# Performance work log

Measured on AMD Instinct MI355X. Metric: run time of the kernel, lower is better.

The kernel has to match this reference:

```python
import jax, jax.numpy as jnp
import numpy as np

N_NODES = 100000
N_EDGES = 3200000
NFEAT = 256
NHID = 256


def setup_inputs() -> dict:
    key = jax.random.key(0)
    k_x, k_ws, k_wn, k_src, k_dst = jax.random.split(key, 5)
    x = jax.random.normal(k_x, (N_NODES, NFEAT), dtype=jnp.float32)
    W_self = jax.random.normal(k_ws, (NFEAT, NHID), dtype=jnp.float32) * (1.0 / np.sqrt(NFEAT))
    W_neigh = jax.random.normal(k_wn, (NFEAT, NHID), dtype=jnp.float32) * (1.0 / np.sqrt(NFEAT))
    b = jnp.zeros((NHID,), dtype=jnp.float32)
    edge_src = jax.random.randint(k_src, (N_EDGES,), 0, N_NODES, dtype=jnp.int32)
    edge_dst = jax.random.randint(k_dst, (N_EDGES,), 0, N_NODES, dtype=jnp.int32)
    return {"x": x, "W_self": W_self, "W_neigh": W_neigh, "b": b,
            "edge_src": edge_src, "edge_dst": edge_dst}


def reference(x, W_self, W_neigh, b, edge_src, edge_dst):
    n = x.shape[0]
    # mean aggregation over incoming edges: gather src feats, scatter-add to dst
    msg = x[edge_src]                                              # [E, F]
    agg = jax.ops.segment_sum(msg, edge_dst, num_segments=n)       # [N, F]
    deg = jax.ops.segment_sum(jnp.ones_like(edge_dst, dtype=x.dtype),
                              edge_dst, num_segments=n)            # [N]
    h_neigh = agg / jnp.maximum(deg, 1.0)[:, None]                 # mean (0 for isolated)
    # SAGEConv 'mean': fc_self(x) + fc_neigh(h_neigh) (bias on neigh branch)
    out = x @ W_self + h_neigh @ W_neigh + b                       # [N, H]
    return jax.nn.relu(out)
```

## Files before the change

### kernel.cpp

```cpp
#include <hip/hip_runtime.h>
#include <stdint.h>

typedef __attribute__((ext_vector_type(8))) short bf16x8;
typedef __attribute__((ext_vector_type(4))) float f32x4;
typedef __attribute__((ext_vector_type(2))) float f32x2;

#define NF 256
#define NH 256
#define KTOT 512
#define BM 128
#define BK 64
#define EB 512
#define NBIN 512

static __device__ __forceinline__ unsigned short f2bf(float f){
  union { float f; unsigned int u; } v; v.f = f;
  unsigned int r = v.u + 0x7fffu + ((v.u >> 16) & 1u);
  return (unsigned short)(r >> 16);
}
static __device__ __forceinline__ unsigned int f2e4(float f){
  union { float f; unsigned int u; } v; v.f = f;
  unsigned int s = v.u >> 31;
  unsigned int mag = v.u & 0x7fffffffu;
  if (mag > 0x43E00000u) mag = 0x43E00000u;
  unsigned int r = mag + 0x7ffffu + ((mag >> 20) & 1u);
  if (r < 0x3C800000u) return 0u;
  return (s << 7) | (((r >> 20) - 960u) & 0x7fu);
}
static __device__ __forceinline__ ushort4 dec8(unsigned int v){
#if __has_builtin(__builtin_amdgcn_cvt_pk_f32_fp8)
  f32x2 lo = __builtin_amdgcn_cvt_pk_f32_fp8((int)v, false);
  f32x2 hi = __builtin_amdgcn_cvt_pk_f32_fp8((int)v, true);
  ushort4 o; o.x=f2bf(lo[0]); o.y=f2bf(lo[1]); o.z=f2bf(hi[0]); o.w=f2bf(hi[1]);
  return o;
#else
  ushort4 o; unsigned short r[4];
  #pragma unroll
  for (int j = 0; j < 4; j++){
    unsigned int b = (v >> (8*j)) & 0xffu;
    unsigned int tt = b & 0x7fu;
    union { unsigned int u; float f; } w;
    w.u = ((tt + 960u) << 20) | ((b & 0x80u) << 24);
    r[j] = tt ? f2bf(w.f) : (unsigned short)0;
  }
  o.x=r[0]; o.y=r[1]; o.z=r[2]; o.w=r[3];
  return o;
#endif
}
static __device__ __forceinline__ void accw(unsigned int v, f32x2& a, f32x2& b){
#if __has_builtin(__builtin_amdgcn_cvt_pk_f32_fp8)
  a += __builtin_amdgcn_cvt_pk_f32_fp8((int)v, false);
  b += __builtin_amdgcn_cvt_pk_f32_fp8((int)v, true);
#else
  #pragma unroll
  for (int j = 0; j < 4; j++){
    unsigned int bb = (v >> (8*j)) & 0xffu;
    unsigned int tt = bb & 0x7fu;
    union { unsigned int u; float f; } w;
    w.u = ((tt + 960u) << 20) | ((bb & 0x80u) << 24);
    float f = tt ? w.f : 0.f;
    if (j==0) a[0] += f; else if (j==1) a[1] += f; else if (j==2) b[0] += f; else b[1] += f;
  }
#endif
}
static __device__ __forceinline__ unsigned int pkw(f32x2 a, f32x2 b){
#if __has_builtin(__builtin_amdgcn_cvt_pk_fp8_f32)
  int t = __builtin_amdgcn_cvt_pk_fp8_f32(a[0], a[1], 0, false);
  t = __builtin_amdgcn_cvt_pk_fp8_f32(b[0], b[1], t, true);
  return (unsigned int)t;
#else
  return f2e4(a[0]) | (f2e4(a[1])<<8) | (f2e4(b[0])<<16) | (f2e4(b[1])<<24);
#endif
}
static __device__ __forceinline__ void gload16(const void* g, void* lds_wave_base, int lane){
#if __has_builtin(__builtin_amdgcn_global_load_lds)
  __builtin_amdgcn_global_load_lds(
      (const __attribute__((address_space(1))) unsigned int*)g,
      (__attribute__((address_space(3))) unsigned int*)lds_wave_base, 16, 0, 0);
  (void)lane;
#else
  *(int4*)((char*)lds_wave_base + (size_t)lane*16) = *(const int4*)g;
#endif
}

__global__ void __launch_bounds__(256) k_cvt(const float* __restrict__ x,
                      unsigned short* __restrict__ xb,
                      unsigned int* __restrict__ xq, int n8,
                      const float* __restrict__ Ws, const float* __restrict__ Wn,
                      unsigned short* __restrict__ Wt,
                      const int* __restrict__ edst, int* __restrict__ H, int ne){
  if (blockIdx.x < 2048){
    for (int i = blockIdx.x*blockDim.x + threadIdx.x; i < n8; i += 2048*blockDim.x){
      const float4* p = (const float4*)(x + (size_t)i*8);
      float4 a = p[0], b = p[1];
      ushort4 o0, o1;
      o0.x=f2bf(a.x); o0.y=f2bf(a.y); o0.z=f2bf(a.z); o0.w=f2bf(a.w);
      o1.x=f2bf(b.x); o1.y=f2bf(b.y); o1.z=f2bf(b.z); o1.w=f2bf(b.w);
      ushort4* q = (ushort4*)(xb + (size_t)i*8);
      q[0] = o0; q[1] = o1;
      unsigned int w0 = f2e4(a.x) | (f2e4(a.y)<<8) | (f2e4(a.z)<<16) | (f2e4(a.w)<<24);
      unsigned int w1 = f2e4(b.x) | (f2e4(b.y)<<8) | (f2e4(b.z)<<16) | (f2e4(b.w)<<24);
      uint2 o; o.x = w0; o.y = w1;
      ((uint2*)xq)[i] = o;
    }
  } else if (blockIdx.x < 2560){
    int t = (blockIdx.x - 2048)*blockDim.x + threadIdx.x;
    if (t < NH*KTOT){
      int n = t >> 9, k = t & 511;
      float v = (k < NF) ? Ws[(size_t)k*NH + n] : Wn[(size_t)(k-NF)*NH + n];
      Wt[t] = (unsigned short)f2bf(v);
    }
  } else {
    __shared__ int lh[NBIN];
    int blk = blockIdx.x - 2560, t = threadIdx.x;
    for (int i = t; i < NBIN; i += 256) lh[i] = 0;
    __syncthreads();
    int chunk = (ne + EB - 1) / EB;
    int e0 = blk * chunk, e1 = ne < e0 + chunk ? ne : e0 + chunk;
    for (int e = e0 + t; e < e1; e += 256)
      atomicAdd(&lh[((unsigned)edst[e]) >> 8], 1);
    __syncthreads();
    for (int i = t; i < NBIN; i += 256) H[i*EB + blk] = lh[i];
  }
}

__global__ void k_partial(const int* __restrict__ deg, int* __restrict__ partial, int n){
  __shared__ int sm[256];
  int b = blockIdx.x, t = threadIdx.x;
  int i0 = b*1024 + t*4;
  int s = 0;
  if (i0 + 3 < n){ int4 v = *(const int4*)(deg + i0); s = v.x+v.y+v.z+v.w; }
  else { for (int j=0;j<4;j++) if (i0+j < n) s += deg[i0+j]; }
  sm[t] = s; __syncthreads();
  for (int d = 128; d > 0; d >>= 1){ if (t < d) sm[t] += sm[t+d]; __syncthreads(); }
  if (t == 0) partial[b] = sm[0];
}

__global__ void k_scanp(int* __restrict__ partial, int nb){
  __shared__ int sm[256];
  int t = threadIdx.x;
  int v = (t < nb) ? partial[t] : 0;
  sm[t] = v; __syncthreads();
  for (int d = 1; d < 256; d <<= 1){
    int u = (t >= d) ? sm[t-d] : 0; __syncthreads();
    sm[t] += u; __syncthreads();
  }
  if (t < nb) partial[t] = sm[t] - v;
}

__global__ void k_scanapply(const int* __restrict__ deg, const int* __restrict__ partial,
                            int* __restrict__ off, int n, int ne){
  __shared__ int sm[256];
  int b = blockIdx.x, t = threadIdx.x;
  int i0 = b*1024 + t*4;
  int d0=0,d1=0,d2=0,d3=0;
  if (i0 + 3 < n){ int4 v = *(const int4*)(deg + i0); d0=v.x; d1=v.y; d2=v.z; d3=v.w; }
  else { if(i0<n)d0=deg[i0]; if(i0+1<n)d1=deg[i0+1]; if(i0+2<n)d2=deg[i0+2]; if(i0+3<n)d3=deg[i0+3]; }
  int s = d0+d1+d2+d3;
  sm[t] = s; __syncthreads();
  for (int d = 1; d < 256; d <<= 1){
    int u = (t >= d) ? sm[t-d] : 0; __syncthreads();
    sm[t] += u; __syncthreads();
  }
  int run = partial[b] + sm[t] - s;
  if (i0   < n) off[i0]   = run; run += d0;
  if (i0+1 < n) off[i0+1] = run; run += d1;
  if (i0+2 < n) off[i0+2] = run; run += d2;
  if (i0+3 < n) off[i0+3] = run;
  if (b == 0 && t == 0) off[n] = ne;
}

__global__ void __launch_bounds__(256) k_bscat(const int* __restrict__ src,
                                               const int* __restrict__ dst,
                                               const int* __restrict__ base,
                                               unsigned int* __restrict__ bkt, int ne){
  __shared__ int lc[NBIN];
  __shared__ int lb[NBIN];
  int blk = blockIdx.x, t = threadIdx.x;
  for (int i = t; i < NBIN; i += 256){ lc[i] = 0; lb[i] = base[i*EB + blk]; }
  __syncthreads();
  int chunk = (ne + EB - 1) / EB;
  int e0 = blk * chunk, e1 = ne < e0 + chunk ? ne : e0 + chunk;
  for (int e = e0 + t; e < e1; e += 256){
    int d = dst[e];
    int bin = ((unsigned)d) >> 8;
    int p = lb[bin] + atomicAdd(&lc[bin], 1);
    bkt[p] = (((unsigned)src[e]) << 8) | ((unsigned)d & 255u);
  }
}

__global__ void __launch_bounds__(256) k_csr(const unsigned int* __restrict__ bkt,
                                             const int* __restrict__ base,
                                             int* __restrict__ off, int* __restrict__ col,
                                             int nn, int ne){
  __shared__ int lh[256], sc[256], se[256], lc[256];
  int b = blockIdx.x, t = threadIdx.x;
  int n0 = base[b*EB], n1 = base[(b+1)*EB];
  lh[t] = 0; lc[t] = 0;
  __syncthreads();
  for (int e = n0 + t; e < n1; e += 256)
    atomicAdd(&lh[bkt[e] & 255u], 1);
  __syncthreads();
  int v = lh[t];
  sc[t] = v; __syncthreads();
  for (int d = 1; d < 256; d <<= 1){
    int u = (t >= d) ? sc[t-d] : 0; __syncthreads();
    sc[t] += u; __syncthreads();
  }
  int excl = sc[t] - v;
  se[t] = excl;
  int node = b*256 + t;
  if (node <= nn) off[node] = n0 + excl;
  __syncthreads();
  for (int e = n0 + t; e < n1; e += 256){
    unsigned u = bkt[e];
    int low = (int)(u & 255u);
    int r = atomicAdd(&lc[low], 1);
    col[n0 + se[low] + r] = (int)(u >> 8);
  }
}

__global__ void __launch_bounds__(256) k_agg(const unsigned int* __restrict__ xw,
                                             const int* __restrict__ off,
                                             const int* __restrict__ col,
                                             unsigned int* __restrict__ hq, int n){
  int w = threadIdx.x >> 6;
  int lane = threadIdx.x & 63;
  int node = blockIdx.x*4 + w;
  if (node >= n) return;
  int e0 = off[node], e1 = off[node+1];
  int deg = e1 - e0;
  f32x2 alo = (f32x2){0.f,0.f}, ahi = (f32x2){0.f,0.f};
  for (int c0 = 0; c0 < deg; c0 += 64){
    int len = deg - c0; if (len > 64) len = 64;
    int cv = 0;
    if (lane < len) cv = col[e0 + c0 + lane];
    int i = 0;
    for (; i + 16 <= len; i += 16){
      unsigned int u[16];
      #pragma unroll
      for (int j = 0; j < 16; j++){
        int s = __builtin_amdgcn_readlane(cv, i + j);
        u[j] = xw[(size_t)s*64 + lane];
      }
      #pragma unroll
      for (int j = 0; j < 16; j++) accw(u[j], alo, ahi);
    }
    for (; i + 4 <= len; i += 4){
      unsigned int u[4];
      #pragma unroll
      for (int j = 0; j < 4; j++){
        int s = __builtin_amdgcn_readlane(cv, i + j);
        u[j] = xw[(size_t)s*64 + lane];
      }
      #pragma unroll
      for (int j = 0; j < 4; j++) accw(u[j], alo, ahi);
    }
    for (; i < len; ++i){
      int s = __builtin_amdgcn_readlane(cv, i);
      unsigned int u0 = xw[(size_t)s*64 + lane];
      accw(u0, alo, ahi);
    }
  }
  float inv = 1.f / (float)(deg > 1 ? deg : 1);
  alo *= inv; ahi *= inv;
  hq[(size_t)node*64 + lane] = pkw(alo, ahi);
}

__global__ void __launch_bounds__(512, 4) k_gemm(const unsigned short* __restrict__ xb,
                                                 const unsigned char*  __restrict__ hq,
                                                 const unsigned short* __restrict__ Wt,
                                                 const float* __restrict__ bias,
                                                 float* __restrict__ out, int M){
  __shared__ __align__(16) unsigned short As[BM*BK];
  __shared__ __align__(16) unsigned short Bs[NH*BK];
  int t = threadIdx.x;
  int m0 = blockIdx.x * BM;
  int w = t >> 6, lane = t & 63;
  int wm = w >> 2, wn = w & 3;
  int lrow = lane & 15;
  int cgrp = (lane >> 4) * 16;
  int slot  = t & 7;

  f32x4 acc[4][4];
  #pragma unroll
  for (int i=0;i<4;i++)
    #pragma unroll
    for (int j=0;j<4;j++) acc[i][j] = (f32x4){0.f,0.f,0.f,0.f};

  for (int kk = 0; kk < KTOT; kk += BK){
    __syncthreads();
    if (kk < NF){
      #pragma unroll
      for (int p = 0; p < 2; p++){
        int flat = p*512 + t;
        int row = flat >> 3;
        const char* g = (const char*)(xb + (size_t)(m0 + row)*NF + kk)
                        + ((slot ^ (row & 7)) << 4);
        gload16(g, (char*)As + (size_t)(flat & ~63)*16, lane);
      }
    } else {
      #pragma unroll
      for (int p = 0; p < 2; p++){
        int flat = p*512 + t;
        int row = flat >> 3;
        const unsigned char* g = hq + (size_t)(m0 + row)*NF + (kk - NF)
                                 + ((slot ^ (row & 7)) << 3);
        uint2 v = *(const uint2*)g;
        ushort4 lo = dec8(v.x), hi = dec8(v.y);
        char* dstb = (char*)As + (size_t)row*128 + slot*16;
        *(ushort4*)dstb = lo;
        *(ushort4*)(dstb + 8) = hi;
      }
    }
    #pragma unroll
    for (int q = 0; q < 4; q++){
      int flat = q*512 + t;
      int row = flat >> 3;
      const char* g = (const char*)(Wt + (size_t)row*KTOT + kk)
                      + ((slot ^ (row & 7)) << 4);
      gload16(g, (char*)Bs + (size_t)(flat & ~63)*16, lane);
    }
    __syncthreads();

    #pragma unroll
    for (int ks = 0; ks < 2; ks++){
      bf16x8 af[4], bfr[4];
      #pragma unroll
      for (int mi=0;mi<4;mi++){
        int row = wm*64 + mi*16 + lrow;
        int cb = (ks*64 + cgrp) ^ ((row & 7) << 4);
        af[mi] = *(const bf16x8*)((const char*)As + (size_t)row*128 + cb);
      }
      #pragma unroll
      for (int ni=0;ni<4;ni++){
        int row = wn*64 + ni*16 + lrow;
        int cb = (ks*64 + cgrp) ^ ((row & 7) << 4);
        bfr[ni] = *(const bf16x8*)((const char*)Bs + (size_t)row*128 + cb);
      }
      #pragma unroll
      for (int mi=0;mi<4;mi++)
        #pragma unroll
        for (int ni=0;ni<4;ni++)
          acc[mi][ni] = __builtin_amdgcn_mfma_f32_16x16x32_bf16(af[mi], bfr[ni], acc[mi][ni], 0, 0, 0);
    }
  }

  #pragma unroll
  for (int ni=0;ni<4;ni++){
    int cn = wn*64 + ni*16 + lrow;
    float bv = bias[cn];
    #pragma unroll
    for (int mi=0;mi<4;mi++){
      #pragma unroll
      for (int r=0;r<4;r++){
        int rm = m0 + wm*64 + mi*16 + (lane>>4)*4 + r;
        if (rm < M){
          float v = acc[mi][ni][r] + bv;
          out[(size_t)rm*NH + cn] = v > 0.f ? v : 0.f;
        }
      }
    }
  }
}

extern "C" void kernel_launch(void* const* d_in, const int* in_sizes, int n_in,
                              void* d_out, int out_size, void* d_ws, size_t ws_size,
                              hipStream_t stream){
  const float* x      = (const float*)d_in[0];
  const float* Wself  = (const float*)d_in[1];
  const float* Wneigh = (const float*)d_in[2];
  const float* bias   = (const float*)d_in[3];
  const int*   esrc   = (const int*)d_in[4];
  const int*   edst   = (const int*)d_in[5];
  const int nn = in_sizes[0] / NF;
  const int ne = in_sizes[4];
  const int mpad = ((nn + BM - 1) / BM) * BM;

  char* w = (char*)d_ws;
  auto alloc = [&](size_t bytes)->char*{
    char* p = w; w += (bytes + 511) & ~size_t(511); return p;
  };
  unsigned short* xb  = (unsigned short*)alloc((size_t)mpad*NF*2);
  unsigned char*  xq  = (unsigned char*)alloc((size_t)nn*NF);
  char* hq_bkt        = alloc((size_t)mpad*NF);
  int* col            = (int*)alloc((size_t)ne*4);
  int* base           = (int*)alloc(((size_t)NBIN*EB + 1)*4);
  int* off            = (int*)alloc((size_t)(nn+1)*4);
  unsigned short* Wt  = (unsigned short*)alloc((size_t)NH*KTOT*2);
  int* partial        = (int*)alloc(4096);
  unsigned int* bkt   = (unsigned int*)hq_bkt;
  unsigned char* hq   = (unsigned char*)hq_bkt;
  int* H              = col;

  const int nH = NBIN*EB;
  const int nb = nH / 1024;

  k_cvt<<<2048 + 512 + 512, 256, 0, stream>>>(x, xb, (unsigned int*)xq, nn*NF/8,
                                              Wself, Wneigh, Wt, edst, H, ne);
  k_partial<<<nb, 256, 0, stream>>>(H, partial, nH);
  k_scanp<<<1, 256, 0, stream>>>(partial, nb);
  k_scanapply<<<nb, 256, 0, stream>>>(H, partial, base, nH, ne);
  k_bscat<<<EB, 256, 0, stream>>>(esrc, edst, base, bkt, ne);
  k_csr<<<NBIN, 256, 0, stream>>>(bkt, base, off, col, nn, ne);
  k_agg<<<(nn + 3)/4, 256, 0, stream>>>((const unsigned int*)xq, off, col, (unsigned int*)hq, nn);
  k_gemm<<<mpad/BM, 512, 0, stream>>>(xb, hq, Wt, bias, (float*)d_out, nn);
}
```

Baseline: 304.1 us.

## Fuse neighbor aggregation into GEMM kernel via shared-memory staging

Merges the per-node mean aggregation kernel into the GEMM kernel. Each 512-thread block first aggregates its 128 nodes' neighbor features into a 32KB shared buffer of packed 8-bit values, then reads that buffer instead of a global hq array during the neighbor half of K. This removes one kernel launch and the global write and read of the aggregated features, at the cost of more shared memory per block (lower occupancy) and a serial gather phase that no longer overlaps with MFMA work. Work distribution also changes, from 25k small blocks to about 782 large ones, so degree imbalance can stall whole blocks.

```diff
diff --git a/kernel.cpp b/kernel.cpp
--- a/kernel.cpp
+++ b/kernel.cpp
@@ -220,63 +220,66 @@
   }
 }
 
-__global__ void __launch_bounds__(256) k_agg(const unsigned int* __restrict__ xw,
-                                             const int* __restrict__ off,
-                                             const int* __restrict__ col,
-                                             unsigned int* __restrict__ hq, int n){
-  int w = threadIdx.x >> 6;
-  int lane = threadIdx.x & 63;
-  int node = blockIdx.x*4 + w;
-  if (node >= n) return;
-  int e0 = off[node], e1 = off[node+1];
-  int deg = e1 - e0;
-  f32x2 alo = (f32x2){0.f,0.f}, ahi = (f32x2){0.f,0.f};
-  for (int c0 = 0; c0 < deg; c0 += 64){
-    int len = deg - c0; if (len > 64) len = 64;
-    int cv = 0;
-    if (lane < len) cv = col[e0 + c0 + lane];
-    int i = 0;
-    for (; i + 16 <= len; i += 16){
-      unsigned int u[16];
-      #pragma unroll
-      for (int j = 0; j < 16; j++){
-        int s = __builtin_amdgcn_readlane(cv, i + j);
-        u[j] = xw[(size_t)s*64 + lane];
-      }
-      #pragma unroll
-      for (int j = 0; j < 16; j++) accw(u[j], alo, ahi);
-    }
-    for (; i + 4 <= len; i += 4){
-      unsigned int u[4];
-      #pragma unroll
-      for (int j = 0; j < 4; j++){
-        int s = __builtin_amdgcn_readlane(cv, i + j);
-        u[j] = xw[(size_t)s*64 + lane];
-      }
-      #pragma unroll
-      for (int j = 0; j < 4; j++) accw(u[j], alo, ahi);
-    }
-    for (; i < len; ++i){
-      int s = __builtin_amdgcn_readlane(cv, i);
-      unsigned int u0 = xw[(size_t)s*64 + lane];
-      accw(u0, alo, ahi);
-    }
-  }
-  float inv = 1.f / (float)(deg > 1 ? deg : 1);
-  alo *= inv; ahi *= inv;
-  hq[(size_t)node*64 + lane] = pkw(alo, ahi);
-}
-
-__global__ void __launch_bounds__(512, 4) k_gemm(const unsigned short* __restrict__ xb,
-                                                 const unsigned char*  __restrict__ hq,
-                                                 const unsigned short* __restrict__ Wt,
-                                                 const float* __restrict__ bias,
-                                                 float* __restrict__ out, int M){
+__global__ void __launch_bounds__(512, 4) k_fused(const unsigned int* __restrict__ xw,
+                                                  const int* __restrict__ off,
+                                                  const int* __restrict__ col,
+                                                  const unsigned short* __restrict__ xb,
+                                                  const unsigned short* __restrict__ Wt,
+                                                  const float* __restrict__ bias,
+                                                  float* __restrict__ out, int nn){
   __shared__ __align__(16) unsigned short As[BM*BK];
   __shared__ __align__(16) unsigned short Bs[NH*BK];
+  __shared__ __align__(16) unsigned int  Hs[BM*64];
   int t = threadIdx.x;
   int m0 = blockIdx.x * BM;
   int w = t >> 6, lane = t & 63;
+
+  for (int r = 0; r < 16; ++r){
+    int nl = w*16 + r;
+    int node = m0 + nl;
+    f32x2 alo = (f32x2){0.f,0.f}, ahi = (f32x2){0.f,0.f};
+    int deg = 0;
+    if (node < nn){
+      int e0 = off[node], e1 = off[node+1];
+      deg = e1 - e0;
+      for (int c0 = 0; c0 < deg; c0 += 64){
+        int len = deg - c0; if (len > 64) len = 64;
+        int cv = 0;
+        if (lane < len) cv = col[e0 + c0 + lane];
+        int i = 0;
+        for (; i + 16 <= len; i += 16){
+          unsigned int u[16];
+          #pragma unroll
+          for (int j = 0; j < 16; j++){
+            int s = __builtin_amdgcn_readlane(cv, i + j);
+            u[j] = xw[(size_t)s*64 + lane];
+          }
+          #pragma unroll
+          for (int j = 0; j < 16; j++) accw(u[j], alo, ahi);
+        }
+        for (; i + 4 <= len; i += 4){
+          unsigned int u[4];
+          #pragma unroll
+          for (int j = 0; j < 4; j++){
+            int s = __builtin_amdgcn_readlane(cv, i + j);
+            u[j] = xw[(size_t)s*64 + lane];
+          }
+          #pragma unroll
+          for (int j = 0; j < 4; j++) accw(u[j], alo, ahi);
+        }
+        for (; i < len; ++i){
+          int s = __builtin_amdgcn_readlane(cv, i);
+          unsigned int u0 = xw[(size_t)s*64 + lane];
+          accw(u0, alo, ahi);
+        }
+      }
+    }
+    float inv = 1.f / (float)(deg > 1 ? deg : 1);
+    alo *= inv; ahi *= inv;
+    Hs[nl*64 + lane] = (node < nn) ? pkw(alo, ahi) : 0u;
+  }
+  __syncthreads();
+
   int wm = w >> 2, wn = w & 3;
   int lrow = lane & 15;
   int cgrp = (lane >> 4) * 16;
@@ -304,9 +307,8 @@
       for (int p = 0; p < 2; p++){
         int flat = p*512 + t;
         int row = flat >> 3;
-        const unsigned char* g = hq + (size_t)(m0 + row)*NF + (kk - NF)
-                                 + ((slot ^ (row & 7)) << 3);
-        uint2 v = *(const uint2*)g;
+        int c4 = ((kk - NF) >> 2) + ((slot ^ (row & 7)) << 1);
+        uint2 v = *(const uint2*)&Hs[row*64 + c4];
         ushort4 lo = dec8(v.x), hi = dec8(v.y);
         char* dstb = (char*)As + (size_t)row*128 + slot*16;
         *(ushort4*)dstb = lo;
@@ -355,7 +357,7 @@
       #pragma unroll
       for (int r=0;r<4;r++){
         int rm = m0 + wm*64 + mi*16 + (lane>>4)*4 + r;
-        if (rm < M){
+        if (rm < nn){
           float v = acc[mi][ni][r] + bv;
           out[(size_t)rm*NH + cn] = v > 0.f ? v : 0.f;
         }
@@ -383,14 +385,12 @@
   };
   unsigned short* xb  = (unsigned short*)alloc((size_t)mpad*NF*2);
   unsigned char*  xq  = (unsigned char*)alloc((size_t)nn*NF);
-  char* hq_bkt        = alloc((size_t)mpad*NF);
+  unsigned int* bkt   = (unsigned int*)alloc((size_t)ne*4);
   int* col            = (int*)alloc((size_t)ne*4);
   int* base           = (int*)alloc(((size_t)NBIN*EB + 1)*4);
   int* off            = (int*)alloc((size_t)(nn+1)*4);
   unsigned short* Wt  = (unsigned short*)alloc((size_t)NH*KTOT*2);
   int* partial        = (int*)alloc(4096);
-  unsigned int* bkt   = (unsigned int*)hq_bkt;
-  unsigned char* hq   = (unsigned char*)hq_bkt;
   int* H              = col;
 
   const int nH = NBIN*EB;
@@ -403,6 +403,6 @@
   k_scanapply<<<nb, 256, 0, stream>>>(H, partial, base, nH, ne);
   k_bscat<<<EB, 256, 0, stream>>>(esrc, edst, base, bkt, ne);
   k_csr<<<NBIN, 256, 0, stream>>>(bkt, base, off, col, nn, ne);
-  k_agg<<<(nn + 3)/4, 256, 0, stream>>>((const unsigned int*)xq, off, col, (unsigned int*)hq, nn);
-  k_gemm<<<mpad/BM, 512, 0, stream>>>(xb, hq, Wt, bias, (float*)d_out, nn);
-}
+  k_fused<<<mpad/BM, 512, 0, stream>>>((const unsigned int*)xq, off, col, xb, Wt, bias,
+                                       (float*)d_out, nn);
+}
```

After: 312.0 us. +2.6%, slower.
